# Performance work log

Hardware: AMD Instinct MI355X
Metric: run time of the kernel (lower is better)

## Reference

```python
import jax, jax.numpy as jnp
import numpy as np
from jax import lax

N_RAYS, N_STEPS, G = 4096, 160, 160
COLOR_DIM, WIDTH = 3, 128
POS_PE, VIEW_PE = 5, 4
XYZ_MIN, XYZ_MAX = -1.0, 1.0
NEAR = 0.05
STEPSIZE = 0.5
VOXEL_SIZE = (XYZ_MAX - XYZ_MIN) / G
DIST = STEPSIZE * VOXEL_SIZE
S_VAL = 80.0
FASTCOLOR_THRES = 1e-7
MASK_THRES = 1e-3
ALPHA_INIT = 1e-4
ACT_SHIFT = float(np.log(1.0 / (1.0 - ALPHA_INIT) - 1.0))
SMOOTH_K, SMOOTH_SIGMA = 5, 1.0
POSFREQ = jnp.asarray([2.0 ** i for i in range(POS_PE)], jnp.float32)
VIEWFREQ = jnp.asarray([2.0 ** i for i in range(VIEW_PE)], jnp.float32)


def _gauss_kernel():
    ax = np.arange(SMOOTH_K) - SMOOTH_K // 2
    g = np.exp(-(ax ** 2) / (2.0 * SMOOTH_SIGMA ** 2))
    k = g[:, None, None] * g[None, :, None] * g[None, None, :]
    return jnp.asarray(k / k.sum(), np.float32)[None, None]


def _trilerp(grid, pts):
    # grid [C,Gx,Gx,Gx]; pts [...,3] in world coords -> [..., C] (align_corners trilinear)
    Gx = grid.shape[-1]
    u = (pts - XYZ_MIN) / (XYZ_MAX - XYZ_MIN) * (Gx - 1)
    u = jnp.clip(u, 0.0, Gx - 1.0)
    i0 = jnp.clip(jnp.floor(u).astype(jnp.int32), 0, Gx - 2)
    f = u - i0.astype(u.dtype)
    x0, y0, z0 = i0[..., 0], i0[..., 1], i0[..., 2]
    fx, fy, fz = f[..., 0], f[..., 1], f[..., 2]
    def g8(ix, iy, iz):
        return grid[:, ix, iy, iz]  # [C, ...]
    out = (g8(x0, y0, z0) * (1 - fx) * (1 - fy) * (1 - fz)
         + g8(x0, y0, z0 + 1) * (1 - fx) * (1 - fy) * fz
         + g8(x0, y0 + 1, z0) * (1 - fx) * fy * (1 - fz)
         + g8(x0, y0 + 1, z0 + 1) * (1 - fx) * fy * fz
         + g8(x0 + 1, y0, z0) * fx * (1 - fy) * (1 - fz)
         + g8(x0 + 1, y0, z0 + 1) * fx * (1 - fy) * fz
         + g8(x0 + 1, y0 + 1, z0) * fx * fy * (1 - fz)
         + g8(x0 + 1, y0 + 1, z0 + 1) * fx * fy * fz)
    return jnp.moveaxis(out, 0, -1)


def _alphas2weights(alpha):
    # per-ray (segmented) exclusive cumprod of transmittance; alpha [N,S]
    T = jnp.cumprod(1.0 - alpha, axis=1)
    T_excl = jnp.concatenate([jnp.ones_like(T[:, :1]), T[:, :-1]], axis=1)
    return alpha * T_excl, T[:, -1]


def _mlp(x, w0, b0, w1, b1, w2, b2):
    h = jax.nn.relu(x @ w0 + b0)
    h = jax.nn.relu(h @ w1 + b1)
    return h @ w2 + b2


def _forward(rays_o, rays_d, viewdirs, sdf_grid, mask_density,
             off_color_grid, emo_color_grid,
             off_w0, off_b0, off_w1, off_b1, off_w2, off_b2,
             emo_w0, emo_b0, emo_w1, emo_b1, emo_w2, emo_b2, em_modes):
    N = rays_o.shape[0]
    t = NEAR + DIST * jnp.arange(N_STEPS, dtype=jnp.float32)
    ray_pts = rays_o[:, None, :] + rays_d[:, None, :] * t[None, :, None]  # [N,S,3]

    # MaskCache: threshold alpha from coarse density grid (boolean keep mask)
    dens = _trilerp(mask_density, ray_pts)[..., 0]
    mask_alpha = 1.0 - jnp.exp(-jax.nn.softplus(dens + ACT_SHIFT) * DIST)
    keep0 = mask_alpha >= MASK_THRES  # [N,S]

    # Gaussian-smoothed SDF grid + central-difference gradient grid
    sdf_s = lax.conv_general_dilated(sdf_grid, _gauss_kernel(), (1, 1, 1), 'SAME',
                                     dimension_numbers=('NCDHW', 'OIDHW', 'NCDHW'))[0]  # [1,G,G,G]
    s = sdf_s[0]
    grad_grid = jnp.zeros((3, G, G, G), sdf_grid.dtype)
    grad_grid = grad_grid.at[0, 1:-1].set((s[2:] - s[:-2]) / (2 * VOXEL_SIZE))
    grad_grid = grad_grid.at[1, :, 1:-1].set((s[:, 2:] - s[:, :-2]) / (2 * VOXEL_SIZE))
    grad_grid = grad_grid.at[2, :, :, 1:-1].set((s[:, :, 2:] - s[:, :, :-2]) / (2 * VOXEL_SIZE))

    sdf = _trilerp(sdf_s, ray_pts)[..., 0]   # [N,S]
    gradient = _trilerp(grad_grid, ray_pts)  # [N,S,3]

    # NeuS alpha from sdf (scatter, grad variant, cos_anneal = 1)
    true_cos = jnp.einsum('nd,nsd->ns', viewdirs, gradient)
    iter_cos = -jax.nn.relu(-true_cos)
    prev_cdf = jax.nn.sigmoid((sdf - iter_cos * DIST * 0.5) * S_VAL)
    next_cdf = jax.nn.sigmoid((sdf + iter_cos * DIST * 0.5) * S_VAL)
    alpha = jnp.clip((prev_cdf - next_cdf + 1e-5) / (prev_cdf + 1e-5), 0.0, 1.0)
    alpha = jnp.where(keep0, alpha, 0.0)  # masked points contribute nothing

    weights, _ = _alphas2weights(alpha)
    keep1 = weights > FASTCOLOR_THRES
    alpha = jnp.where(keep1, alpha, 0.0)
    weights, alphainv_last = _alphas2weights(alpha)

    # features: pos PE, view PE (per-ray, gathered by ray_id == broadcast), normal
    rays_xyz = (ray_pts - XYZ_MIN) / (XYZ_MAX - XYZ_MIN)  # [N,S,3]
    xyz_emb = (rays_xyz[..., None] * POSFREQ).reshape(N, N_STEPS, -1)
    v_emb = (viewdirs[..., None] * VIEWFREQ).reshape(N, -1)
    v_full = jnp.concatenate([v_emb, jnp.sin(v_emb), jnp.cos(v_emb)], -1)
    v_full = jnp.broadcast_to(v_full[:, None, :], (N, N_STEPS, v_full.shape[-1]))
    normal = gradient / (jnp.linalg.norm(gradient, axis=-1, keepdims=True) + 1e-5)
    rgb_feat = jnp.concatenate([rays_xyz, jnp.sin(xyz_emb), jnp.cos(xyz_emb), v_full, normal], -1)

    off_in = jnp.concatenate([_trilerp(off_color_grid, ray_pts), rgb_feat], -1)
    emo_in = jnp.concatenate([_trilerp(emo_color_grid, ray_pts), rgb_feat], -1)
    off_rgb = jax.nn.sigmoid(_mlp(off_in, off_w0, off_b0, off_w1, off_b1, off_w2, off_b2))
    emo_rgb = jax.nn.sigmoid(_mlp(emo_in, emo_w0, emo_b0, emo_w1, emo_b1, emo_w2, emo_b2))
    on_mask = (em_modes == 1)[:, None, None]  # em_modes[ray_id] == 1
    rgb = jnp.where(on_mask, emo_rgb, 0.0) + off_rgb

    w_ = weights[..., None]
    rgb_marched = jnp.sum(w_ * rgb, axis=1)  # segment_coo(sum over ray_id)
    cum_weights = jnp.sum(w_, axis=1)        # [N,1]
    return rgb_marched, alphainv_last, 1.0 - cum_weights


def setup_inputs() -> dict:
    key = jax.random.key(0)
    ks = jax.random.split(key, 12)
    rays_o = jax.random.uniform(ks[0], (N_RAYS, 3), jnp.float32, -0.3, 0.3)
    rd = jax.random.normal(ks[1], (N_RAYS, 3), jnp.float32)
    rays_d = rd / jnp.linalg.norm(rd, axis=-1, keepdims=True)
    viewdirs = rays_d
    em_modes = jax.random.randint(ks[2], (N_RAYS,), 0, 2)
    lin = np.linspace(-1.0, 1.0, G, dtype=np.float32)
    x, y, z = np.meshgrid(lin, lin, lin, indexing='ij')
    sdf_grid = jnp.asarray(np.sqrt(x ** 2 + y ** 2 + z ** 2) - 1.0)[None, None]  # sphere-SDF init
    mask_density = jax.random.normal(ks[3], (1, 80, 80, 80), jnp.float32) * 2.0 + 12.0
    off_color_grid = jax.random.normal(ks[4], (COLOR_DIM, G, G, G), jnp.float32) * 0.1
    emo_color_grid = jax.random.normal(ks[5], (COLOR_DIM, G, G, G), jnp.float32) * 0.1
    DIM0 = 3 + 3 * POS_PE * 2 + 3 * VIEW_PE * 3 + COLOR_DIM + 3  # = 75
    def lw(k, i, o):
        return jax.random.normal(k, (i, o), jnp.float32) * (1.0 / np.sqrt(i))
    return dict(rays_o=rays_o, rays_d=rays_d, viewdirs=viewdirs, em_modes=em_modes,
                sdf_grid=sdf_grid, mask_density=mask_density,
                off_color_grid=off_color_grid, emo_color_grid=emo_color_grid,
                off_w0=lw(ks[6], DIM0, WIDTH), off_b0=jnp.zeros((WIDTH,), jnp.float32),
                off_w1=lw(ks[7], WIDTH, WIDTH), off_b1=jnp.zeros((WIDTH,), jnp.float32),
                off_w2=lw(ks[8], WIDTH, 3), off_b2=jnp.zeros((3,), jnp.float32),
                emo_w0=lw(ks[9], DIM0, WIDTH), emo_b0=jnp.zeros((WIDTH,), jnp.float32),
                emo_w1=lw(ks[10], WIDTH, WIDTH), emo_b1=jnp.zeros((WIDTH,), jnp.float32),
                emo_w2=lw(ks[11], WIDTH, 3), emo_b2=jnp.zeros((3,), jnp.float32))


def reference(rays_o, rays_d, viewdirs, em_modes, sdf_grid, mask_density,
              off_color_grid, emo_color_grid,
              off_w0, off_b0, off_w1, off_b1, off_w2, off_b2,
              emo_w0, emo_b0, emo_w1, emo_b1, emo_w2, emo_b2):
    return _forward(rays_o, rays_d, viewdirs, sdf_grid, mask_density,
                    off_color_grid, emo_color_grid,
                    off_w0, off_b0, off_w1, off_b1, off_w2, off_b2,
                    emo_w0, emo_b0, emo_w1, emo_b1, emo_w2, emo_b2, em_modes)
```

## Files before the change

kernel.cpp:

```cpp
#include <hip/hip_runtime.h>

#define NRAYS 4096
#define NSTEPS 160
#define NSAMP (NRAYS*NSTEPS)
#define GG 160
#define GG2 (GG*GG)
#define GG3 (GG*GG2)
#define GM 80
#define GM2 (GM*GM)

#define NEARV 0.05f
#define DISTV 0.00625f
#define SVAL 80.0f
#define ACT_SHIFT_C (-9.2102403669758813f)
#define INV2H 40.0f
#define MASK_THRES_C 1e-3f
#define FAST_THRES_C 1e-7f

#define KW0 0.05448868454964295f
#define KW1 0.24420134200323332f
#define KW2 0.40261994689424750f

__device__ __forceinline__ float sigmf(float x){ return 1.0f/(1.0f+__expf(-x)); }
__device__ __forceinline__ float softplusf_(float x){ return (x>20.0f)? x : log1pf(__expf(x)); }

__device__ __forceinline__ void tricoord(float p, int Gx, int& i0, float& fr){
  float u = (p + 1.0f)*0.5f*(float)(Gx-1);
  u = fminf(fmaxf(u, 0.0f), (float)(Gx-1));
  int i = (int)floorf(u);
  i = min(max(i,0), Gx-2);
  i0 = i; fr = u - (float)i;
}

__global__ __launch_bounds__(256) void ksmooth_yz(const float* __restrict__ in, float* __restrict__ out,
                                                  float* __restrict__ outbuf, int* __restrict__ cnt){
  __shared__ float S[36][37];
  __shared__ float Tz[36][33];
  const int bx = blockIdx.x;
  const int t = threadIdx.x;
  if (bx == 0){
    for (int i = t; i < NRAYS*3; i += 256) outbuf[i] = 0.0f;
    if (t < 2) cnt[t] = 0;
  }
  const int x  = bx / 25;
  const int tile = bx % 25;
  const int Y0 = (tile/5)*32, Z0 = (tile%5)*32;
  const float kw[5] = {KW0,KW1,KW2,KW1,KW0};
  for (int i = t; i < 36*36; i += 256){
    int r = i/36, c = i - (i/36)*36;
    int y = Y0 + r - 2, z = Z0 + c - 2;
    float v = 0.0f;
    if (y>=0 && y<GG && z>=0 && z<GG) v = in[(x*GG+y)*GG+z];
    S[r][c] = v;
  }
  __syncthreads();
  for (int i = t; i < 36*32; i += 256){
    int r = i >> 5, c = i & 31;
    float acc = 0.f;
    #pragma unroll
    for (int d=0; d<5; d++) acc += kw[d]*S[r][c+d];
    Tz[r][c] = acc;
  }
  __syncthreads();
  for (int i = t; i < 32*32; i += 256){
    int yy = i >> 5, c = i & 31;
    float acc = 0.f;
    #pragma unroll
    for (int d=0; d<5; d++) acc += kw[d]*Tz[yy+d][c];
    out[(x*GG + Y0+yy)*GG + Z0 + c] = acc;
  }
}

__global__ __launch_bounds__(64) void kmarch(
  const float* __restrict__ ro, const float* __restrict__ rd,
  const float* __restrict__ vd, const int* __restrict__ em,
  const float* __restrict__ maskg, const float* __restrict__ Y,
  int* __restrict__ slist, float* __restrict__ sw, float* __restrict__ sgrad,
  int* __restrict__ cnt, float* __restrict__ out)
{
  int n = blockIdx.x*64 + threadIdx.x;
  if (n >= NRAYS) return;
  const float ox=ro[n*3+0], oy=ro[n*3+1], oz=ro[n*3+2];
  const float dx=rd[n*3+0], dy=rd[n*3+1], dz=rd[n*3+2];
  const float vx=vd[n*3+0], vy=vd[n*3+1], vz=vd[n*3+2];
  const int emn = em[n];
  const float kwc[5] = {KW0,KW1,KW2,KW1,KW0};
  float T1=1.0f, T2=1.0f, cum=0.0f;
  for (int s=0; s<NSTEPS; s++){
    float tt = NEARV + DISTV*(float)s;
    float px = ox + dx*tt, py = oy + dy*tt, pz = oz + dz*tt;

    int mx,my,mz; float mfx,mfy,mfz;
    tricoord(px, GM, mx, mfx); tricoord(py, GM, my, mfy); tricoord(pz, GM, mz, mfz);
    int mid = (mx*GM + my)*GM + mz;
    float d000=maskg[mid],        d001=maskg[mid+1];
    float d010=maskg[mid+GM],     d011=maskg[mid+GM+1];
    float d100=maskg[mid+GM2],    d101=maskg[mid+GM2+1];
    float d110=maskg[mid+GM2+GM], d111=maskg[mid+GM2+GM+1];
    float m00 = d000 + (d001-d000)*mfz;
    float m01 = d010 + (d011-d010)*mfz;
    float m10 = d100 + (d101-d100)*mfz;
    float m11 = d110 + (d111-d110)*mfz;
    float m0 = m00 + (m01-m00)*mfy;
    float m1 = m10 + (m11-m10)*mfy;
    float dens = m0 + (m1-m0)*mfx;
    float malpha = 1.0f - __expf(-softplusf_(dens + ACT_SHIFT_C)*DISTV);

    int ix,iy,iz; float fx,fy,fz;
    tricoord(px, GG, ix, fx); tricoord(py, GG, iy, fy); tricoord(pz, GG, iz, fz);

    float R[2][2][8];
    #pragma unroll
    for (int jb=0;jb<2;jb++)
      #pragma unroll
      for (int jc=0;jc<2;jc++)
        #pragma unroll
        for (int j=0;j<8;j++){
          int a = ix-3+j;
          R[jb][jc][j] = (a>=0 && a<GG) ? Y[(a*GG + iy+jb)*GG + iz+jc] : 0.0f;
        }
    const bool hasym = (iy>=1), hasyp = (iy<=GG-3);
    const bool haszm = (iz>=1), haszp = (iz<=GG-3);
    float Eym[2][6], Eyp[2][6], Ezm[2][6], Ezp[2][6];
    #pragma unroll
    for (int jc=0;jc<2;jc++)
      #pragma unroll
      for (int j=0;j<6;j++){
        int a = ix-2+j;
        bool ax = (a>=0 && a<GG);
        Eym[jc][j] = (hasym && ax) ? Y[(a*GG + iy-1)*GG + iz+jc] : 0.0f;
        Eyp[jc][j] = (hasyp && ax) ? Y[(a*GG + iy+2)*GG + iz+jc] : 0.0f;
      }
    #pragma unroll
    for (int jb=0;jb<2;jb++)
      #pragma unroll
      for (int j=0;j<6;j++){
        int a = ix-2+j;
        bool ax = (a>=0 && a<GG);
        Ezm[jb][j] = (haszm && ax) ? Y[(a*GG + iy+jb)*GG + iz-1] : 0.0f;
        Ezp[jb][j] = (haszp && ax) ? Y[(a*GG + iy+jb)*GG + iz+2] : 0.0f;
      }

    float sdf=0.0f, gx=0.0f, gy=0.0f, gz=0.0f;
    #pragma unroll
    for (int ja=0;ja<2;ja++){
      #pragma unroll
      for (int jb=0;jb<2;jb++){
        #pragma unroll
        for (int jc=0;jc<2;jc++){
          float w = (ja?fx:1.0f-fx)*(jb?fy:1.0f-fy)*(jc?fz:1.0f-fz);
          const float* r = R[jb][jc];
          float s0=0.0f;
          #pragma unroll
          for (int t2=0;t2<5;t2++) s0 += kwc[t2]*r[ja+1+t2];
          sdf += w*s0;
          int a = ix+ja, b = iy+jb, c = iz+jc;
          if (a>=1 && a<=GG-2){
            float sp=0.0f, sm=0.0f;
            #pragma unroll
            for (int t2=0;t2<5;t2++){ sp += kwc[t2]*r[ja+2+t2]; sm += kwc[t2]*r[ja+t2]; }
            gx += w*INV2H*(sp-sm);
          }
          if (b>=1 && b<=GG-2){
            float acc=0.0f;
            if (jb==0){
              const float* up = R[1][jc];
              const float* dn = Eym[jc];
              #pragma unroll
              for (int t2=0;t2<5;t2++) acc += kwc[t2]*(up[ja+1+t2] - dn[ja+t2]);
            } else {
              const float* up = Eyp[jc];
              const float* dn = R[0][jc];
              #pragma unroll
              for (int t2=0;t2<5;t2++) acc += kwc[t2]*(up[ja+t2] - dn[ja+1+t2]);
            }
            gy += w*INV2H*acc;
          }
          if (c>=1 && c<=GG-2){
            float acc=0.0f;
            if (jc==0){
              const float* up = R[jb][1];
              const float* dn = Ezm[jb];
              #pragma unroll
              for (int t2=0;t2<5;t2++) acc += kwc[t2]*(up[ja+1+t2] - dn[ja+t2]);
            } else {
              const float* up = Ezp[jb];
              const float* dn = R[jb][0];
              #pragma unroll
              for (int t2=0;t2<5;t2++) acc += kwc[t2]*(up[ja+t2] - dn[ja+1+t2]);
            }
            gz += w*INV2H*acc;
          }
        }
      }
    }

    float tc = vx*gx + vy*gy + vz*gz;
    float icos = fminf(tc, 0.0f);
    float e = icos*DISTV*0.5f;
    float prev = sigmf((sdf - e)*SVAL);
    float nxt  = sigmf((sdf + e)*SVAL);
    float alpha = (prev - nxt + 1e-5f)/(prev + 1e-5f);
    alpha = fminf(fmaxf(alpha, 0.0f), 1.0f);
    if (!(malpha >= MASK_THRES_C)) alpha = 0.0f;

    float w1 = alpha*T1; T1 *= (1.0f - alpha);
    float a2 = (w1 > FAST_THRES_C) ? alpha : 0.0f;
    float wv = a2*T2;   T2 *= (1.0f - a2);
    cum += wv;
    if (wv > 0.0f){
      int pos;
      if (emn == 1){ int p = atomicAdd(&cnt[1], 1); pos = NSAMP - 1 - p; }
      else         { pos = atomicAdd(&cnt[0], 1); }
      slist[pos] = n*NSTEPS + s;
      sw[pos] = wv;
      sgrad[pos*3+0]=gx; sgrad[pos*3+1]=gy; sgrad[pos*3+2]=gz;
    }
    if (T1 <= FAST_THRES_C) break;
  }
  out[NRAYS*3 + n] = T2;
  out[NRAYS*4 + n] = 1.0f - cum;
}

__global__ __launch_bounds__(256) void kmlp7(
  const float* __restrict__ ro, const float* __restrict__ rd,
  const float* __restrict__ vd,
  const float* __restrict__ offc, const float* __restrict__ emoc,
  const int* __restrict__ slist, const float* __restrict__ sw,
  const float* __restrict__ sgrad, const int* __restrict__ cnt,
  const float* __restrict__ W0o, const float* __restrict__ b0o,
  const float* __restrict__ W1o, const float* __restrict__ b1o,
  const float* __restrict__ W2o, const float* __restrict__ b2o,
  const float* __restrict__ W0e, const float* __restrict__ b0e,
  const float* __restrict__ W1e, const float* __restrict__ b1e,
  const float* __restrict__ W2e, const float* __restrict__ b2e,
  float* __restrict__ out)
{
  __shared__ float X[4][2][80];
  __shared__ float H[4][2][128];

  const int t = threadIdx.x;
  const int wid = t >> 6;
  const int lt  = t & 63;
  const int c0 = cnt[0], c1 = cnt[1];
  const int seg1 = NSAMP - c1;
  const int totOff = c0 + c1;
  const int nOff = (totOff + 1) >> 1;
  const int nEmo = (c1 + 1) >> 1;
  const int nTask = nOff + nEmo;

  for (int task = blockIdx.x*4 + wid; task < nTask; task += gridDim.x*4) {
    const int head = (task >= nOff) ? 1 : 0;
    const int total = head ? c1 : totOff;
    const int v0 = (head ? (task - nOff) : task) * 2;

    const float* W0 = head ? W0e : W0o;  const float* b0 = head ? b0e : b0o;
    const float* W1 = head ? W1e : W1o;  const float* b1 = head ? b1e : b1o;
    const float* W2 = head ? W2e : W2o;  const float* b2 = head ? b2e : b2o;
    const float* cg = head ? emoc : offc;
    const float4* W04 = (const float4*)W0;
    const float4* W14 = (const float4*)W1;

    int my_i; float my_w; int my_samp;
    {
      int v = v0 + (lt & 1);
      int vc = (v < total) ? v : (total - 1);
      int i = head ? (seg1 + vc) : ((vc < c0) ? vc : seg1 + (vc - c0));
      my_i = i;
      my_samp = slist[i];
      my_w = (v < total) ? sw[i] : 0.0f;
    }
    const int iA = __shfl(my_i, 0, 64),    iB = __shfl(my_i, 1, 64);
    const int sampA = __shfl(my_samp, 0, 64), sampB = __shfl(my_samp, 1, 64);
    const float wgtA = __shfl(my_w, 0, 64),   wgtB = __shfl(my_w, 1, 64);

    {
      const int s = lt & 1;
      const int r = lt >> 1;
      const int samp = s ? sampB : sampA;
      const int gi   = s ? iB : iA;
      const int n = samp / NSTEPS;
      const int step = samp - n*NSTEPS;
      const float tt = NEARV + DISTV*(float)step;
      const float px = ro[n*3+0] + rd[n*3+0]*tt;
      const float py = ro[n*3+1] + rd[n*3+1]*tt;
      const float pz = ro[n*3+2] + rd[n*3+2]*tt;
      if (r < 3) {
        int ix,iy,iz; float fx,fy,fz;
        tricoord(px, GG, ix, fx); tricoord(py, GG, iy, fy); tricoord(pz, GG, iz, fz);
        const float* g = cg + (size_t)r * GG3;
        const int id = (ix*GG + iy)*GG + iz;
        float v000=g[id],        v001=g[id+1];
        float v010=g[id+GG],     v011=g[id+GG+1];
        float v100=g[id+GG2],    v101=g[id+GG2+1];
        float v110=g[id+GG2+GG], v111=g[id+GG2+GG+1];
        float c00 = v000 + (v001-v000)*fz;
        float c01 = v010 + (v011-v010)*fz;
        float c10 = v100 + (v101-v100)*fz;
        float c11 = v110 + (v111-v110)*fz;
        float cl0 = c00 + (c01-c00)*fy;
        float cl1 = c10 + (c11-c10)*fy;
        X[wid][s][r] = cl0 + (cl1-cl0)*fx;
      } else if (r == 3) {
        X[wid][s][3] = (px+1.0f)*0.5f;
        X[wid][s][4] = (py+1.0f)*0.5f;
        X[wid][s][5] = (pz+1.0f)*0.5f;
        float gx = sgrad[gi*3+0], gy = sgrad[gi*3+1], gz = sgrad[gi*3+2];
        float inv = 1.0f/(sqrtf(gx*gx+gy*gy+gz*gz)+1e-5f);
        X[wid][s][72] = gx*inv; X[wid][s][73] = gy*inv; X[wid][s][74] = gz*inv;
        X[wid][s][75] = 0.0f; X[wid][s][76] = 0.0f;
        X[wid][s][77] = 0.0f; X[wid][s][78] = 0.0f; X[wid][s][79] = 0.0f;
      } else if (r < 7) {
        const int a = r - 4;
        const float coord = (a==0)?px:((a==1)?py:pz);
        const float rxyz = (coord+1.0f)*0.5f;
        float fr = 1.0f;
        #pragma unroll
        for (int q = 0; q < 5; q++) {
          float e = rxyz*fr; fr *= 2.0f;
          X[wid][s][6  + a*5 + q] = __sinf(e);
          X[wid][s][21 + a*5 + q] = __cosf(e);
        }
      } else if (r < 10) {
        const int a = r - 7;
        const float v = vd[n*3+a];
        float fr = 1.0f;
        #pragma unroll
        for (int q = 0; q < 4; q++) {
          float e = v*fr; fr *= 2.0f;
          X[wid][s][36 + a*4 + q] = e;
          X[wid][s][48 + a*4 + q] = __sinf(e);
          X[wid][s][60 + a*4 + q] = __cosf(e);
        }
      }
    }

    const int sme = lt >> 5;
    const int l32 = lt & 31;
    const float* Xs = X[wid][sme];
    const float myw = sme ? wgtB : wgtA;
    const int mysamp = sme ? sampB : sampA;

    float4 h4;
    {
      float4 acc = ((const float4*)b0)[l32];
      #pragma unroll 3
      for (int k4 = 0; k4 < 72; k4 += 4){
        float4 w0 = W04[(k4+0)*32 + l32];
        float4 w1 = W04[(k4+1)*32 + l32];
        float4 w2 = W04[(k4+2)*32 + l32];
        float4 w3 = W04[(k4+3)*32 + l32];
        float4 x = *(const float4*)&Xs[k4];
        acc.x+=x.x*w0.x; acc.y+=x.x*w0.y; acc.z+=x.x*w0.z; acc.w+=x.x*w0.w;
        acc.x+=x.y*w1.x; acc.y+=x.y*w1.y; acc.z+=x.y*w1.z; acc.w+=x.y*w1.w;
        acc.x+=x.z*w2.x; acc.y+=x.z*w2.y; acc.z+=x.z*w2.z; acc.w+=x.z*w2.w;
        acc.x+=x.w*w3.x; acc.y+=x.w*w3.y; acc.z+=x.w*w3.z; acc.w+=x.w*w3.w;
      }
      #pragma unroll
      for (int k = 72; k < 75; k++){
        float4 w = W04[k*32 + l32];
        float x = Xs[k];
        acc.x+=x*w.x; acc.y+=x*w.y; acc.z+=x*w.z; acc.w+=x*w.w;
      }
      h4.x = fmaxf(acc.x,0.f); h4.y = fmaxf(acc.y,0.f);
      h4.z = fmaxf(acc.z,0.f); h4.w = fmaxf(acc.w,0.f);
      *(float4*)&H[wid][sme][l32*4] = h4;
    }

    {
      const float* Hs = H[wid][sme];
      float4 acc = ((const float4*)b1)[l32];
      #pragma unroll 4
      for (int k4 = 0; k4 < 128; k4 += 4){
        float4 w0 = W14[(k4+0)*32 + l32];
        float4 w1 = W14[(k4+1)*32 + l32];
        float4 w2 = W14[(k4+2)*32 + l32];
        float4 w3 = W14[(k4+3)*32 + l32];
        float4 x = *(const float4*)&Hs[k4];
        acc.x+=x.x*w0.x; acc.y+=x.x*w0.y; acc.z+=x.x*w0.z; acc.w+=x.x*w0.w;
        acc.x+=x.y*w1.x; acc.y+=x.y*w1.y; acc.z+=x.y*w1.z; acc.w+=x.y*w1.w;
        acc.x+=x.z*w2.x; acc.y+=x.z*w2.y; acc.z+=x.z*w2.z; acc.w+=x.z*w2.w;
        acc.x+=x.w*w3.x; acc.y+=x.w*w3.y; acc.z+=x.w*w3.z; acc.w+=x.w*w3.w;
      }
      h4.x = fmaxf(acc.x,0.f); h4.y = fmaxf(acc.y,0.f);
      h4.z = fmaxf(acc.z,0.f); h4.w = fmaxf(acc.w,0.f);
    }

    {
      float c0v = h4.x*W2[(l32*4+0)*3+0] + h4.y*W2[(l32*4+1)*3+0]
                + h4.z*W2[(l32*4+2)*3+0] + h4.w*W2[(l32*4+3)*3+0];
      float c1v = h4.x*W2[(l32*4+0)*3+1] + h4.y*W2[(l32*4+1)*3+1]
                + h4.z*W2[(l32*4+2)*3+1] + h4.w*W2[(l32*4+3)*3+1];
      float c2v = h4.x*W2[(l32*4+0)*3+2] + h4.y*W2[(l32*4+1)*3+2]
                + h4.z*W2[(l32*4+2)*3+2] + h4.w*W2[(l32*4+3)*3+2];
      #pragma unroll
      for (int d=16; d>=1; d>>=1){
        c0v += __shfl_down(c0v, d, 32);
        c1v += __shfl_down(c1v, d, 32);
        c2v += __shfl_down(c2v, d, 32);
      }
      if (l32 == 0 && myw > 0.0f){
        int n2 = mysamp / NSTEPS;
        atomicAdd(&out[n2*3+0], myw * sigmf(c0v + b2[0]));
        atomicAdd(&out[n2*3+1], myw * sigmf(c1v + b2[1]));
        atomicAdd(&out[n2*3+2], myw * sigmf(c2v + b2[2]));
      }
    }
  }
}

extern "C" void kernel_launch(void* const* d_in, const int* in_sizes, int n_in,
                              void* d_out, int out_size, void* d_ws, size_t ws_size,
                              hipStream_t stream) {
  const float* ro    = (const float*)d_in[0];
  const float* rd    = (const float*)d_in[1];
  const float* vd    = (const float*)d_in[2];
  const int*   em    = (const int*)d_in[3];
  const float* sdfg  = (const float*)d_in[4];
  const float* maskg = (const float*)d_in[5];
  const float* offc  = (const float*)d_in[6];
  const float* emoc  = (const float*)d_in[7];
  const float* W0o = (const float*)d_in[8];
  const float* b0o = (const float*)d_in[9];
  const float* W1o = (const float*)d_in[10];
  const float* b1o = (const float*)d_in[11];
  const float* W2o = (const float*)d_in[12];
  const float* b2o = (const float*)d_in[13];
  const float* W0e = (const float*)d_in[14];
  const float* b0e = (const float*)d_in[15];
  const float* W1e = (const float*)d_in[16];
  const float* b1e = (const float*)d_in[17];
  const float* W2e = (const float*)d_in[18];
  const float* b2e = (const float*)d_in[19];

  float* out = (float*)d_out;
  float* ws  = (float*)d_ws;
  float* Yb    = ws;
  float* swb   = ws + GG3;
  float* sgradb= swb + NSAMP;
  int*   slist = (int*)(sgradb + 3*(size_t)NSAMP);
  int*   cnt   = slist + NSAMP;

  ksmooth_yz<<<GG*25, 256, 0, stream>>>(sdfg, Yb, out, cnt);

  kmarch<<<NRAYS/64, 64, 0, stream>>>(ro, rd, vd, em, maskg, Yb,
                                      slist, swb, sgradb, cnt, out);

  kmlp7<<<1024, 256, 0, stream>>>(ro, rd, vd, offc, emoc,
                                  slist, swb, sgradb, cnt,
                                  W0o,b0o,W1o,b1o,W2o,b2o,
                                  W0e,b0e,W1e,b1e,W2e,b2e, out);
}
```

Baseline: 60.66 us.

## Batch eight samples per wave in MLP and process march steps in pairs

The MLP kernel now assigns eight samples per wavefront instead of two, so each half-wave accumulates four samples at once and reuses every loaded weight float4 four times. Sample weights and ids are staged in shared memory and the output layer is looped per sample. The march loop evaluates two steps' geometry before the serial transmittance update, trying to expose more memory-level parallelism, at the cost of possibly computing one extra step past early termination and higher register pressure. Launch bounds add a minimum-blocks hint and the MLP grid shrinks to 256 blocks.

```diff
diff --git a/kernel.cpp b/kernel.cpp
--- a/kernel.cpp
+++ b/kernel.cpp
@@ -71,7 +71,129 @@
   }
 }
 
-__global__ __launch_bounds__(64) void kmarch(
+__device__ __forceinline__ void geom_step(
+  float px, float py, float pz, float vx, float vy, float vz,
+  const float* __restrict__ maskg, const float* __restrict__ Y,
+  float& alpha_o, float& gx_o, float& gy_o, float& gz_o)
+{
+  const float kwc[5] = {KW0,KW1,KW2,KW1,KW0};
+  int mx,my,mz; float mfx,mfy,mfz;
+  tricoord(px, GM, mx, mfx); tricoord(py, GM, my, mfy); tricoord(pz, GM, mz, mfz);
+  int mid = (mx*GM + my)*GM + mz;
+  float d000=maskg[mid],        d001=maskg[mid+1];
+  float d010=maskg[mid+GM],     d011=maskg[mid+GM+1];
+  float d100=maskg[mid+GM2],    d101=maskg[mid+GM2+1];
+  float d110=maskg[mid+GM2+GM], d111=maskg[mid+GM2+GM+1];
+  float m00 = d000 + (d001-d000)*mfz;
+  float m01 = d010 + (d011-d010)*mfz;
+  float m10 = d100 + (d101-d100)*mfz;
+  float m11 = d110 + (d111-d110)*mfz;
+  float m0 = m00 + (m01-m00)*mfy;
+  float m1 = m10 + (m11-m10)*mfy;
+  float dens = m0 + (m1-m0)*mfx;
+  float malpha = 1.0f - __expf(-softplusf_(dens + ACT_SHIFT_C)*DISTV);
+
+  int ix,iy,iz; float fx,fy,fz;
+  tricoord(px, GG, ix, fx); tricoord(py, GG, iy, fy); tricoord(pz, GG, iz, fz);
+
+  float R[2][2][8];
+  #pragma unroll
+  for (int jb=0;jb<2;jb++)
+    #pragma unroll
+    for (int jc=0;jc<2;jc++)
+      #pragma unroll
+      for (int j=0;j<8;j++){
+        int a = ix-3+j;
+        R[jb][jc][j] = (a>=0 && a<GG) ? Y[(a*GG + iy+jb)*GG + iz+jc] : 0.0f;
+      }
+  const bool hasym = (iy>=1), hasyp = (iy<=GG-3);
+  const bool haszm = (iz>=1), haszp = (iz<=GG-3);
+  float Eym[2][6], Eyp[2][6], Ezm[2][6], Ezp[2][6];
+  #pragma unroll
+  for (int jc=0;jc<2;jc++)
+    #pragma unroll
+    for (int j=0;j<6;j++){
+      int a = ix-2+j;
+      bool ax = (a>=0 && a<GG);
+      Eym[jc][j] = (hasym && ax) ? Y[(a*GG + iy-1)*GG + iz+jc] : 0.0f;
+      Eyp[jc][j] = (hasyp && ax) ? Y[(a*GG + iy+2)*GG + iz+jc] : 0.0f;
+    }
+  #pragma unroll
+  for (int jb=0;jb<2;jb++)
+    #pragma unroll
+    for (int j=0;j<6;j++){
+      int a = ix-2+j;
+      bool ax = (a>=0 && a<GG);
+      Ezm[jb][j] = (haszm && ax) ? Y[(a*GG + iy+jb)*GG + iz-1] : 0.0f;
+      Ezp[jb][j] = (haszp && ax) ? Y[(a*GG + iy+jb)*GG + iz+2] : 0.0f;
+    }
+
+  float sdf=0.0f, gx=0.0f, gy=0.0f, gz=0.0f;
+  #pragma unroll
+  for (int ja=0;ja<2;ja++){
+    #pragma unroll
+    for (int jb=0;jb<2;jb++){
+      #pragma unroll
+      for (int jc=0;jc<2;jc++){
+        float w = (ja?fx:1.0f-fx)*(jb?fy:1.0f-fy)*(jc?fz:1.0f-fz);
+        const float* r = R[jb][jc];
+        float s0=0.0f;
+        #pragma unroll
+        for (int t2=0;t2<5;t2++) s0 += kwc[t2]*r[ja+1+t2];
+        sdf += w*s0;
+        int a = ix+ja, b = iy+jb, c = iz+jc;
+        if (a>=1 && a<=GG-2){
+          float sp=0.0f, sm=0.0f;
+          #pragma unroll
+          for (int t2=0;t2<5;t2++){ sp += kwc[t2]*r[ja+2+t2]; sm += kwc[t2]*r[ja+t2]; }
+          gx += w*INV2H*(sp-sm);
+        }
+        if (b>=1 && b<=GG-2){
+          float acc=0.0f;
+          if (jb==0){
+            const float* up = R[1][jc];
+            const float* dn = Eym[jc];
+            #pragma unroll
+            for (int t2=0;t2<5;t2++) acc += kwc[t2]*(up[ja+1+t2] - dn[ja+t2]);
+          } else {
+            const float* up = Eyp[jc];
+            const float* dn = R[0][jc];
+            #pragma unroll
+            for (int t2=0;t2<5;t2++) acc += kwc[t2]*(up[ja+t2] - dn[ja+1+t2]);
+          }
+          gy += w*INV2H*acc;
+        }
+        if (c>=1 && c<=GG-2){
+          float acc=0.0f;
+          if (jc==0){
+            const float* up = R[jb][1];
+            const float* dn = Ezm[jb];
+            #pragma unroll
+            for (int t2=0;t2<5;t2++) acc += kwc[t2]*(up[ja+1+t2] - dn[ja+t2]);
+          } else {
+            const float* up = Ezp[jb];
+            const float* dn = R[jb][0];
+            #pragma unroll
+            for (int t2=0;t2<5;t2++) acc += kwc[t2]*(up[ja+t2] - dn[ja+1+t2]);
+          }
+          gz += w*INV2H*acc;
+        }
+      }
+    }
+  }
+
+  float tc = vx*gx + vy*gy + vz*gz;
+  float icos = fminf(tc, 0.0f);
+  float e = icos*DISTV*0.5f;
+  float prev = sigmf((sdf - e)*SVAL);
+  float nxt  = sigmf((sdf + e)*SVAL);
+  float alpha = (prev - nxt + 1e-5f)/(prev + 1e-5f);
+  alpha = fminf(fmaxf(alpha, 0.0f), 1.0f);
+  if (!(malpha >= MASK_THRES_C)) alpha = 0.0f;
+  alpha_o = alpha; gx_o = gx; gy_o = gy; gz_o = gz;
+}
+
+__global__ __launch_bounds__(64, 1) void kmarch(
   const float* __restrict__ ro, const float* __restrict__ rd,
   const float* __restrict__ vd, const int* __restrict__ em,
   const float* __restrict__ maskg, const float* __restrict__ Y,
@@ -84,137 +206,31 @@
   const float dx=rd[n*3+0], dy=rd[n*3+1], dz=rd[n*3+2];
   const float vx=vd[n*3+0], vy=vd[n*3+1], vz=vd[n*3+2];
   const int emn = em[n];
-  const float kwc[5] = {KW0,KW1,KW2,KW1,KW0};
   float T1=1.0f, T2=1.0f, cum=0.0f;
-  for (int s=0; s<NSTEPS; s++){
-    float tt = NEARV + DISTV*(float)s;
-    float px = ox + dx*tt, py = oy + dy*tt, pz = oz + dz*tt;
-
-    int mx,my,mz; float mfx,mfy,mfz;
-    tricoord(px, GM, mx, mfx); tricoord(py, GM, my, mfy); tricoord(pz, GM, mz, mfz);
-    int mid = (mx*GM + my)*GM + mz;
-    float d000=maskg[mid],        d001=maskg[mid+1];
-    float d010=maskg[mid+GM],     d011=maskg[mid+GM+1];
-    float d100=maskg[mid+GM2],    d101=maskg[mid+GM2+1];
-    float d110=maskg[mid+GM2+GM], d111=maskg[mid+GM2+GM+1];
-    float m00 = d000 + (d001-d000)*mfz;
-    float m01 = d010 + (d011-d010)*mfz;
-    float m10 = d100 + (d101-d100)*mfz;
-    float m11 = d110 + (d111-d110)*mfz;
-    float m0 = m00 + (m01-m00)*mfy;
-    float m1 = m10 + (m11-m10)*mfy;
-    float dens = m0 + (m1-m0)*mfx;
-    float malpha = 1.0f - __expf(-softplusf_(dens + ACT_SHIFT_C)*DISTV);
-
-    int ix,iy,iz; float fx,fy,fz;
-    tricoord(px, GG, ix, fx); tricoord(py, GG, iy, fy); tricoord(pz, GG, iz, fz);
-
-    float R[2][2][8];
-    #pragma unroll
-    for (int jb=0;jb<2;jb++)
-      #pragma unroll
-      for (int jc=0;jc<2;jc++)
-        #pragma unroll
-        for (int j=0;j<8;j++){
-          int a = ix-3+j;
-          R[jb][jc][j] = (a>=0 && a<GG) ? Y[(a*GG + iy+jb)*GG + iz+jc] : 0.0f;
-        }
-    const bool hasym = (iy>=1), hasyp = (iy<=GG-3);
-    const bool haszm = (iz>=1), haszp = (iz<=GG-3);
-    float Eym[2][6], Eyp[2][6], Ezm[2][6], Ezp[2][6];
-    #pragma unroll
-    for (int jc=0;jc<2;jc++)
-      #pragma unroll
-      for (int j=0;j<6;j++){
-        int a = ix-2+j;
-        bool ax = (a>=0 && a<GG);
-        Eym[jc][j] = (hasym && ax) ? Y[(a*GG + iy-1)*GG + iz+jc] : 0.0f;
-        Eyp[jc][j] = (hasyp && ax) ? Y[(a*GG + iy+2)*GG + iz+jc] : 0.0f;
-      }
-    #pragma unroll
-    for (int jb=0;jb<2;jb++)
-      #pragma unroll
-      for (int j=0;j<6;j++){
-        int a = ix-2+j;
-        bool ax = (a>=0 && a<GG);
-        Ezm[jb][j] = (haszm && ax) ? Y[(a*GG + iy+jb)*GG + iz-1] : 0.0f;
-        Ezp[jb][j] = (haszp && ax) ? Y[(a*GG + iy+jb)*GG + iz+2] : 0.0f;
-      }
-
-    float sdf=0.0f, gx=0.0f, gy=0.0f, gz=0.0f;
-    #pragma unroll
-    for (int ja=0;ja<2;ja++){
-      #pragma unroll
-      for (int jb=0;jb<2;jb++){
-        #pragma unroll
-        for (int jc=0;jc<2;jc++){
-          float w = (ja?fx:1.0f-fx)*(jb?fy:1.0f-fy)*(jc?fz:1.0f-fz);
-          const float* r = R[jb][jc];
-          float s0=0.0f;
-          #pragma unroll
-          for (int t2=0;t2<5;t2++) s0 += kwc[t2]*r[ja+1+t2];
-          sdf += w*s0;
-          int a = ix+ja, b = iy+jb, c = iz+jc;
-          if (a>=1 && a<=GG-2){
-            float sp=0.0f, sm=0.0f;
-            #pragma unroll
-            for (int t2=0;t2<5;t2++){ sp += kwc[t2]*r[ja+2+t2]; sm += kwc[t2]*r[ja+t2]; }
-            gx += w*INV2H*(sp-sm);
-          }
-          if (b>=1 && b<=GG-2){
-            float acc=0.0f;
-            if (jb==0){
-              const float* up = R[1][jc];
-              const float* dn = Eym[jc];
-              #pragma unroll
-              for (int t2=0;t2<5;t2++) acc += kwc[t2]*(up[ja+1+t2] - dn[ja+t2]);
-            } else {
-              const float* up = Eyp[jc];
-              const float* dn = R[0][jc];
-              #pragma unroll
-              for (int t2=0;t2<5;t2++) acc += kwc[t2]*(up[ja+t2] - dn[ja+1+t2]);
-            }
-            gy += w*INV2H*acc;
-          }
-          if (c>=1 && c<=GG-2){
-            float acc=0.0f;
-            if (jc==0){
-              const float* up = R[jb][1];
-              const float* dn = Ezm[jb];
-              #pragma unroll
-              for (int t2=0;t2<5;t2++) acc += kwc[t2]*(up[ja+1+t2] - dn[ja+t2]);
-            } else {
-              const float* up = Ezp[jb];
-              const float* dn = R[jb][0];
-              #pragma unroll
-              for (int t2=0;t2<5;t2++) acc += kwc[t2]*(up[ja+t2] - dn[ja+1+t2]);
-            }
-            gz += w*INV2H*acc;
-          }
-        }
-      }
-    }
-
-    float tc = vx*gx + vy*gy + vz*gz;
-    float icos = fminf(tc, 0.0f);
-    float e = icos*DISTV*0.5f;
-    float prev = sigmf((sdf - e)*SVAL);
-    float nxt  = sigmf((sdf + e)*SVAL);
-    float alpha = (prev - nxt + 1e-5f)/(prev + 1e-5f);
-    alpha = fminf(fmaxf(alpha, 0.0f), 1.0f);
-    if (!(malpha >= MASK_THRES_C)) alpha = 0.0f;
-
-    float w1 = alpha*T1; T1 *= (1.0f - alpha);
-    float a2 = (w1 > FAST_THRES_C) ? alpha : 0.0f;
-    float wv = a2*T2;   T2 *= (1.0f - a2);
-    cum += wv;
-    if (wv > 0.0f){
-      int pos;
-      if (emn == 1){ int p = atomicAdd(&cnt[1], 1); pos = NSAMP - 1 - p; }
-      else         { pos = atomicAdd(&cnt[0], 1); }
-      slist[pos] = n*NSTEPS + s;
-      sw[pos] = wv;
-      sgrad[pos*3+0]=gx; sgrad[pos*3+1]=gy; sgrad[pos*3+2]=gz;
+  for (int c = 0; c < NSTEPS/2; c++){
+    float av[2], gxa[2], gya[2], gza[2];
+    #pragma unroll
+    for (int j = 0; j < 2; j++){
+      const int s = c*2 + j;
+      const float tt = NEARV + DISTV*(float)s;
+      geom_step(ox + dx*tt, oy + dy*tt, oz + dz*tt, vx, vy, vz,
+                maskg, Y, av[j], gxa[j], gya[j], gza[j]);
+    }
+    #pragma unroll
+    for (int j = 0; j < 2; j++){
+      float alpha = av[j];
+      float w1 = alpha*T1; T1 *= (1.0f - alpha);
+      float a2 = (w1 > FAST_THRES_C) ? alpha : 0.0f;
+      float wv = a2*T2;   T2 *= (1.0f - a2);
+      cum += wv;
+      if (wv > 0.0f){
+        int pos;
+        if (emn == 1){ int p = atomicAdd(&cnt[1], 1); pos = NSAMP - 1 - p; }
+        else         { pos = atomicAdd(&cnt[0], 1); }
+        slist[pos] = n*NSTEPS + c*2 + j;
+        sw[pos] = wv;
+        sgrad[pos*3+0]=gxa[j]; sgrad[pos*3+1]=gya[j]; sgrad[pos*3+2]=gza[j];
+      }
     }
     if (T1 <= FAST_THRES_C) break;
   }
@@ -222,7 +238,13 @@
   out[NRAYS*4 + n] = 1.0f - cum;
 }
 
-__global__ __launch_bounds__(256) void kmlp7(
+#define DO4(ACC, XV) \
+  ACC.x += XV.x*w0.x; ACC.y += XV.x*w0.y; ACC.z += XV.x*w0.z; ACC.w += XV.x*w0.w; \
+  ACC.x += XV.y*w1.x; ACC.y += XV.y*w1.y; ACC.z += XV.y*w1.z; ACC.w += XV.y*w1.w; \
+  ACC.x += XV.z*w2.x; ACC.y += XV.z*w2.y; ACC.z += XV.z*w2.z; ACC.w += XV.z*w2.w; \
+  ACC.x += XV.w*w3.x; ACC.y += XV.w*w3.y; ACC.z += XV.w*w3.z; ACC.w += XV.w*w3.w;
+
+__global__ __launch_bounds__(256, 1) void kmlp8(
   const float* __restrict__ ro, const float* __restrict__ rd,
   const float* __restrict__ vd,
   const float* __restrict__ offc, const float* __restrict__ emoc,
@@ -236,8 +258,11 @@
   const float* __restrict__ W2e, const float* __restrict__ b2e,
   float* __restrict__ out)
 {
-  __shared__ float X[4][2][80];
-  __shared__ float H[4][2][128];
+  __shared__ float X [4][8][80];
+  __shared__ float HA[4][8][128];
+  __shared__ float HB[4][8][128];
+  __shared__ float SW_[4][8];
+  __shared__ int   SS_[4][8];
 
   const int t = threadIdx.x;
   const int wid = t >> 6;
@@ -245,14 +270,14 @@
   const int c0 = cnt[0], c1 = cnt[1];
   const int seg1 = NSAMP - c1;
   const int totOff = c0 + c1;
-  const int nOff = (totOff + 1) >> 1;
-  const int nEmo = (c1 + 1) >> 1;
+  const int nOff = (totOff + 7) >> 3;
+  const int nEmo = (c1 + 7) >> 3;
   const int nTask = nOff + nEmo;
 
   for (int task = blockIdx.x*4 + wid; task < nTask; task += gridDim.x*4) {
     const int head = (task >= nOff) ? 1 : 0;
     const int total = head ? c1 : totOff;
-    const int v0 = (head ? (task - nOff) : task) * 2;
+    const int base = (head ? (task - nOff) : task) * 8;
 
     const float* W0 = head ? W0e : W0o;  const float* b0 = head ? b0e : b0o;
     const float* W1 = head ? W1e : W1o;  const float* b1 = head ? b1e : b1o;
@@ -261,30 +286,25 @@
     const float4* W04 = (const float4*)W0;
     const float4* W14 = (const float4*)W1;
 
-    int my_i; float my_w; int my_samp;
     {
-      int v = v0 + (lt & 1);
-      int vc = (v < total) ? v : (total - 1);
-      int i = head ? (seg1 + vc) : ((vc < c0) ? vc : seg1 + (vc - c0));
-      my_i = i;
-      my_samp = slist[i];
-      my_w = (v < total) ? sw[i] : 0.0f;
-    }
-    const int iA = __shfl(my_i, 0, 64),    iB = __shfl(my_i, 1, 64);
-    const int sampA = __shfl(my_samp, 0, 64), sampB = __shfl(my_samp, 1, 64);
-    const float wgtA = __shfl(my_w, 0, 64),   wgtB = __shfl(my_w, 1, 64);
-
-    {
-      const int s = lt & 1;
-      const int r = lt >> 1;
-      const int samp = s ? sampB : sampA;
-      const int gi   = s ? iB : iA;
+      const int s = lt >> 3;
+      const int r = lt & 7;
+      int v = base + s;
+      bool vld = (v < total);
+      int vc = vld ? v : (total > 0 ? total - 1 : 0);
+      int gi = head ? (seg1 + vc) : ((vc < c0) ? vc : seg1 + (vc - c0));
+      const int samp = slist[gi];
+      if (r == 0){
+        SS_[wid][s] = samp;
+        SW_[wid][s] = vld ? sw[gi] : 0.0f;
+      }
       const int n = samp / NSTEPS;
       const int step = samp - n*NSTEPS;
       const float tt = NEARV + DISTV*(float)step;
       const float px = ro[n*3+0] + rd[n*3+0]*tt;
       const float py = ro[n*3+1] + rd[n*3+1]*tt;
       const float pz = ro[n*3+2] + rd[n*3+2]*tt;
+      float* Xs = X[wid][s];
       if (r < 3) {
         int ix,iy,iz; float fx,fy,fz;
         tricoord(px, GG, ix, fx); tricoord(py, GG, iy, fy); tricoord(pz, GG, iz, fz);
@@ -300,16 +320,15 @@
         float c11 = v110 + (v111-v110)*fz;
         float cl0 = c00 + (c01-c00)*fy;
         float cl1 = c10 + (c11-c10)*fy;
-        X[wid][s][r] = cl0 + (cl1-cl0)*fx;
+        Xs[r] = cl0 + (cl1-cl0)*fx;
       } else if (r == 3) {
-        X[wid][s][3] = (px+1.0f)*0.5f;
-        X[wid][s][4] = (py+1.0f)*0.5f;
-        X[wid][s][5] = (pz+1.0f)*0.5f;
+        Xs[3] = (px+1.0f)*0.5f;
+        Xs[4] = (py+1.0f)*0.5f;
+        Xs[5] = (pz+1.0f)*0.5f;
         float gx = sgrad[gi*3+0], gy = sgrad[gi*3+1], gz = sgrad[gi*3+2];
         float inv = 1.0f/(sqrtf(gx*gx+gy*gy+gz*gz)+1e-5f);
-        X[wid][s][72] = gx*inv; X[wid][s][73] = gy*inv; X[wid][s][74] = gz*inv;
-        X[wid][s][75] = 0.0f; X[wid][s][76] = 0.0f;
-        X[wid][s][77] = 0.0f; X[wid][s][78] = 0.0f; X[wid][s][79] = 0.0f;
+        Xs[72] = gx*inv; Xs[73] = gy*inv; Xs[74] = gz*inv;
+        Xs[75] = 0.0f; Xs[76] = 0.0f; Xs[77] = 0.0f; Xs[78] = 0.0f; Xs[79] = 0.0f;
       } else if (r < 7) {
         const int a = r - 4;
         const float coord = (a==0)?px:((a==1)?py:pz);
@@ -318,92 +337,126 @@
         #pragma unroll
         for (int q = 0; q < 5; q++) {
           float e = rxyz*fr; fr *= 2.0f;
-          X[wid][s][6  + a*5 + q] = __sinf(e);
-          X[wid][s][21 + a*5 + q] = __cosf(e);
-        }
-      } else if (r < 10) {
-        const int a = r - 7;
-        const float v = vd[n*3+a];
-        float fr = 1.0f;
+          Xs[6  + a*5 + q] = __sinf(e);
+          Xs[21 + a*5 + q] = __cosf(e);
+        }
+      } else {
         #pragma unroll
-        for (int q = 0; q < 4; q++) {
-          float e = v*fr; fr *= 2.0f;
-          X[wid][s][36 + a*4 + q] = e;
-          X[wid][s][48 + a*4 + q] = __sinf(e);
-          X[wid][s][60 + a*4 + q] = __cosf(e);
+        for (int a = 0; a < 3; a++){
+          const float vv = vd[n*3+a];
+          float fr = 1.0f;
+          #pragma unroll
+          for (int q = 0; q < 4; q++) {
+            float e = vv*fr; fr *= 2.0f;
+            Xs[36 + a*4 + q] = e;
+            Xs[48 + a*4 + q] = __sinf(e);
+            Xs[60 + a*4 + q] = __cosf(e);
+          }
         }
       }
     }
 
     const int sme = lt >> 5;
     const int l32 = lt & 31;
-    const float* Xs = X[wid][sme];
-    const float myw = sme ? wgtB : wgtA;
-    const int mysamp = sme ? sampB : sampA;
-
-    float4 h4;
+    const int sb = sme*4;
+
     {
-      float4 acc = ((const float4*)b0)[l32];
-      #pragma unroll 3
+      const float4 bb = ((const float4*)b0)[l32];
+      float4 a0 = bb, a1 = bb, a2 = bb, a3 = bb;
+      const float* X0 = X[wid][sb+0];
+      const float* X1 = X[wid][sb+1];
+      const float* X2 = X[wid][sb+2];
+      const float* X3 = X[wid][sb+3];
+      #pragma unroll 2
       for (int k4 = 0; k4 < 72; k4 += 4){
         float4 w0 = W04[(k4+0)*32 + l32];
         float4 w1 = W04[(k4+1)*32 + l32];
         float4 w2 = W04[(k4+2)*32 + l32];
         float4 w3 = W04[(k4+3)*32 + l32];
-        float4 x = *(const float4*)&Xs[k4];
-        acc.x+=x.x*w0.x; acc.y+=x.x*w0.y; acc.z+=x.x*w0.z; acc.w+=x.x*w0.w;
-        acc.x+=x.y*w1.x; acc.y+=x.y*w1.y; acc.z+=x.y*w1.z; acc.w+=x.y*w1.w;
-        acc.x+=x.z*w2.x; acc.y+=x.z*w2.y; acc.z+=x.z*w2.z; acc.w+=x.z*w2.w;
-        acc.x+=x.w*w3.x; acc.y+=x.w*w3.y; acc.z+=x.w*w3.z; acc.w+=x.w*w3.w;
+        float4 x0 = *(const float4*)&X0[k4];
+        float4 x1 = *(const float4*)&X1[k4];
+        float4 x2 = *(const float4*)&X2[k4];
+        float4 x3 = *(const float4*)&X3[k4];
+        DO4(a0, x0); DO4(a1, x1); DO4(a2, x2); DO4(a3, x3);
       }
       #pragma unroll
       for (int k = 72; k < 75; k++){
         float4 w = W04[k*32 + l32];
-        float x = Xs[k];
-        acc.x+=x*w.x; acc.y+=x*w.y; acc.z+=x*w.z; acc.w+=x*w.w;
-      }
-      h4.x = fmaxf(acc.x,0.f); h4.y = fmaxf(acc.y,0.f);
-      h4.z = fmaxf(acc.z,0.f); h4.w = fmaxf(acc.w,0.f);
-      *(float4*)&H[wid][sme][l32*4] = h4;
+        float x0 = X0[k], x1 = X1[k], x2 = X2[k], x3 = X3[k];
+        a0.x+=x0*w.x; a0.y+=x0*w.y; a0.z+=x0*w.z; a0.w+=x0*w.w;
+        a1.x+=x1*w.x; a1.y+=x1*w.y; a1.z+=x1*w.z; a1.w+=x1*w.w;
+        a2.x+=x2*w.x; a2.y+=x2*w.y; a2.z+=x2*w.z; a2.w+=x2*w.w;
+        a3.x+=x3*w.x; a3.y+=x3*w.y; a3.z+=x3*w.z; a3.w+=x3*w.w;
+      }
+      a0.x=fmaxf(a0.x,0.f); a0.y=fmaxf(a0.y,0.f); a0.z=fmaxf(a0.z,0.f); a0.w=fmaxf(a0.w,0.f);
+      a1.x=fmaxf(a1.x,0.f); a1.y=fmaxf(a1.y,0.f); a1.z=fmaxf(a1.z,0.f); a1.w=fmaxf(a1.w,0.f);
+      a2.x=fmaxf(a2.x,0.f); a2.y=fmaxf(a2.y,0.f); a2.z=fmaxf(a2.z,0.f); a2.w=fmaxf(a2.w,0.f);
+      a3.x=fmaxf(a3.x,0.f); a3.y=fmaxf(a3.y,0.f); a3.z=fmaxf(a3.z,0.f); a3.w=fmaxf(a3.w,0.f);
+      *(float4*)&HA[wid][sb+0][l32*4] = a0;
+      *(float4*)&HA[wid][sb+1][l32*4] = a1;
+      *(float4*)&HA[wid][sb+2][l32*4] = a2;
+      *(float4*)&HA[wid][sb+3][l32*4] = a3;
     }
 
     {
-      const float* Hs = H[wid][sme];
-      float4 acc = ((const float4*)b1)[l32];
-      #pragma unroll 4
+      const float4 bb = ((const float4*)b1)[l32];
+      float4 a0 = bb, a1 = bb, a2 = bb, a3 = bb;
+      const float* H0 = HA[wid][sb+0];
+      const float* H1 = HA[wid][sb+1];
+      const float* H2p = HA[wid][sb+2];
+      const float* H3 = HA[wid][sb+3];
+      #pragma unroll 2
       for (int k4 = 0; k4 < 128; k4 += 4){
         float4 w0 = W14[(k4+0)*32 + l32];
         float4 w1 = W14[(k4+1)*32 + l32];
         float4 w2 = W14[(k4+2)*32 + l32];
         float4 w3 = W14[(k4+3)*32 + l32];
-        float4 x = *(const float4*)&Hs[k4];
-        acc.x+=x.x*w0.x; acc.y+=x.x*w0.y; acc.z+=x.x*w0.z; acc.w+=x.x*w0.w;
-        acc.x+=x.y*w1.x; acc.y+=x.y*w1.y; acc.z+=x.y*w1.z; acc.w+=x.y*w1.w;
-        acc.x+=x.z*w2.x; acc.y+=x.z*w2.y; acc.z+=x.z*w2.z; acc.w+=x.z*w2.w;
-        acc.x+=x.w*w3.x; acc.y+=x.w*w3.y; acc.z+=x.w*w3.z; acc.w+=x.w*w3.w;
-      }
-      h4.x = fmaxf(acc.x,0.f); h4.y = fmaxf(acc.y,0.f);
-      h4.z = fmaxf(acc.z,0.f); h4.w = fmaxf(acc.w,0.f);
+        float4 x0 = *(const float4*)&H0[k4];
+        float4 x1 = *(const float4*)&H1[k4];
+        float4 x2 = *(const float4*)&H2p[k4];
+        float4 x3 = *(const float4*)&H3[k4];
+        DO4(a0, x0); DO4(a1, x1); DO4(a2, x2); DO4(a3, x3);
+      }
+      a0.x=fmaxf(a0.x,0.f); a0.y=fmaxf(a0.y,0.f); a0.z=fmaxf(a0.z,0.f); a0.w=fmaxf(a0.w,0.f);
+      a1.x=fmaxf(a1.x,0.f); a1.y=fmaxf(a1.y,0.f); a1.z=fmaxf(a1.z,0.f); a1.w=fmaxf(a1.w,0.f);
+      a2.x=fmaxf(a2.x,0.f); a2.y=fmaxf(a2.y,0.f); a2.z=fmaxf(a2.z,0.f); a2.w=fmaxf(a2.w,0.f);
+      a3.x=fmaxf(a3.x,0.f); a3.y=fmaxf(a3.y,0.f); a3.z=fmaxf(a3.z,0.f); a3.w=fmaxf(a3.w,0.f);
+      *(float4*)&HB[wid][sb+0][l32*4] = a0;
+      *(float4*)&HB[wid][sb+1][l32*4] = a1;
+      *(float4*)&HB[wid][sb+2][l32*4] = a2;
+      *(float4*)&HB[wid][sb+3][l32*4] = a3;
     }
 
     {
-      float c0v = h4.x*W2[(l32*4+0)*3+0] + h4.y*W2[(l32*4+1)*3+0]
-                + h4.z*W2[(l32*4+2)*3+0] + h4.w*W2[(l32*4+3)*3+0];
-      float c1v = h4.x*W2[(l32*4+0)*3+1] + h4.y*W2[(l32*4+1)*3+1]
-                + h4.z*W2[(l32*4+2)*3+1] + h4.w*W2[(l32*4+3)*3+1];
-      float c2v = h4.x*W2[(l32*4+0)*3+2] + h4.y*W2[(l32*4+1)*3+2]
-                + h4.z*W2[(l32*4+2)*3+2] + h4.w*W2[(l32*4+3)*3+2];
+      float W2r[4][3];
       #pragma unroll
-      for (int d=16; d>=1; d>>=1){
-        c0v += __shfl_down(c0v, d, 32);
-        c1v += __shfl_down(c1v, d, 32);
-        c2v += __shfl_down(c2v, d, 32);
-      }
-      if (l32 == 0 && myw > 0.0f){
-        int n2 = mysamp / NSTEPS;
-        atomicAdd(&out[n2*3+0], myw * sigmf(c0v + b2[0]));
-        atomicAdd(&out[n2*3+1], myw * sigmf(c1v + b2[1]));
-        atomicAdd(&out[n2*3+2], myw * sigmf(c2v + b2[2]));
+      for (int q = 0; q < 4; q++){
+        W2r[q][0] = W2[(l32*4+q)*3+0];
+        W2r[q][1] = W2[(l32*4+q)*3+1];
+        W2r[q][2] = W2[(l32*4+q)*3+2];
+      }
+      #pragma unroll
+      for (int m = 0; m < 4; m++){
+        const int s = sb + m;
+        float4 h = *(const float4*)&HB[wid][s][l32*4];
+        float c0v = h.x*W2r[0][0] + h.y*W2r[1][0] + h.z*W2r[2][0] + h.w*W2r[3][0];
+        float c1v = h.x*W2r[0][1] + h.y*W2r[1][1] + h.z*W2r[2][1] + h.w*W2r[3][1];
+        float c2v = h.x*W2r[0][2] + h.y*W2r[1][2] + h.z*W2r[2][2] + h.w*W2r[3][2];
+        #pragma unroll
+        for (int d=16; d>=1; d>>=1){
+          c0v += __shfl_down(c0v, d, 32);
+          c1v += __shfl_down(c1v, d, 32);
+          c2v += __shfl_down(c2v, d, 32);
+        }
+        if (l32 == 0){
+          float w = SW_[wid][s];
+          if (w > 0.0f){
+            int n2 = SS_[wid][s] / NSTEPS;
+            atomicAdd(&out[n2*3+0], w * sigmf(c0v + b2[0]));
+            atomicAdd(&out[n2*3+1], w * sigmf(c1v + b2[1]));
+            atomicAdd(&out[n2*3+2], w * sigmf(c2v + b2[2]));
+          }
+        }
       }
     }
   }
@@ -446,8 +499,8 @@
   kmarch<<<NRAYS/64, 64, 0, stream>>>(ro, rd, vd, em, maskg, Yb,
                                       slist, swb, sgradb, cnt, out);
 
-  kmlp7<<<1024, 256, 0, stream>>>(ro, rd, vd, offc, emoc,
-                                  slist, swb, sgradb, cnt,
-                                  W0o,b0o,W1o,b1o,W2o,b2o,
-                                  W0e,b0e,W1e,b1e,W2e,b2e, out);
+  kmlp8<<<256, 256, 0, stream>>>(ro, rd, vd, offc, emoc,
+                                 slist, swb, sgradb, cnt,
+                                 W0o,b0o,W1o,b1o,W2o,b2o,
+                                 W0e,b0e,W1e,b1e,W2e,b2e, out);
 }
```

After: 60.55 us. Within noise of the previous version (-0.2%).
